# Kernel optimization log

Measured on AMD Instinct MI355X. Metric: run time of the kernel, lower is better.

The kernel has to match this reference:

```python
import jax, jax.numpy as jnp
import numpy as np

HIER_WEIGHT = 0.1

def setup_inputs() -> dict:
    key = jax.random.key(0)
    k1, k2, k3, k4, k5 = jax.random.split(key, 5)
    B, N, D = 128, 100000, 256
    E = N - 1
    return {
        "logits": jax.random.normal(k1, (B, N), dtype=jnp.float32),
        "labels": jax.random.randint(k2, (B,), 0, N, dtype=jnp.int64),
        "label_emb": jax.random.normal(k3, (N, D), dtype=jnp.float32),
        "parent_idx": jax.random.randint(k4, (E,), 0, N, dtype=jnp.int64),
        "child_idx": jax.random.randint(k5, (E,), 0, N, dtype=jnp.int64),
    }

def reference(logits, labels, label_emb, parent_idx, child_idx):
    # base loss: mean cross-entropy over the batch (loss_fn)
    logp = jax.nn.log_softmax(logits, axis=-1)                      # [B, N]
    ce = -jnp.take_along_axis(logp, labels[:, None], axis=-1)       # [B, 1]
    base_loss = jnp.mean(ce)
    # hierarchy penalty: sum over all (parent, child) edges of ||p - c||_2^2
    diff = label_emb[parent_idx] - label_emb[child_idx]             # [E, D]
    recursive_loss = jnp.sum(diff * diff)
    return base_loss + HIER_WEIGHT * recursive_loss
```

## Files before the change

kernel.cpp:

```cpp
#include <hip/hip_runtime.h>
#include <math.h>


#define TPB 256
#define WPB (TPB / 64)
#define EB  32
#define CE_SLICES 8

typedef float f32x4 __attribute__((ext_vector_type(4)));

__global__ __launch_bounds__(TPB, 4) void hier_work_kernel(
    const float* __restrict__ logits,
    const float* __restrict__ emb,
    const int* __restrict__ parent,
    const int* __restrict__ child,
    float* __restrict__ ws_edge,
    float* __restrict__ ws_ce,
    int N, int E, int n_edge_blocks)
{
    __shared__ float red[WPB];
    const int tid  = threadIdx.x;
    const int lane = tid & 63;
    const int wv   = tid >> 6;
    const float L2E = 1.4426950408889634f;

    if ((int)blockIdx.x < n_edge_blocks) {
        const int wave = blockIdx.x * WPB + wv;
        const int base = wave * EB;

        float acc = 0.0f;
        if (base < E) {
            const int n = min(EB, E - base);
            int idx = 0;
            if (lane < EB) {
                if (lane < n) idx = parent[base + lane];
            } else {
                const int j = lane - EB;
                if (j < n) idx = child[base + j];
            }
            const float4* __restrict__ emb4 = (const float4*)emb;

            #pragma unroll 4
            for (int j = 0; j < n; ++j) {
                const int p = __shfl(idx, j);
                const int c = __shfl(idx, j + EB);
                float4 a = emb4[(size_t)p * 64 + lane];
                float4 b = emb4[(size_t)c * 64 + lane];
                const float dx = a.x - b.x, dy = a.y - b.y;
                const float dz = a.z - b.z, dw = a.w - b.w;
                acc += dx * dx + dy * dy + dz * dz + dw * dw;
            }
        }

        #pragma unroll
        for (int off = 32; off; off >>= 1) acc += __shfl_xor(acc, off);
        if (lane == 0) red[wv] = acc;
        __syncthreads();
        if (tid == 0) {
            float t = 0.0f;
            #pragma unroll
            for (int k = 0; k < WPB; ++k) t += red[k];
            ws_edge[blockIdx.x] = t;
        }
    } else {
        const int cu    = (int)blockIdx.x - n_edge_blocks;
        const int row   = cu >> 3;
        const int slice = cu & (CE_SLICES - 1);
        const int n4    = N >> 2;
        const int per   = n4 / CE_SLICES;
        const f32x4* __restrict__ rp4 =
            (const f32x4*)(logits + (size_t)row * (size_t)N)
            + (size_t)slice * per;

        float s0 = 0.0f, s1 = 0.0f;
        int i = tid;
        for (; i + TPB < per; i += 2 * TPB) {
            f32x4 v0 = __builtin_nontemporal_load(&rp4[i]);
            f32x4 v1 = __builtin_nontemporal_load(&rp4[i + TPB]);
            s0 += exp2f(v0.x * L2E) + exp2f(v0.y * L2E)
                + exp2f(v0.z * L2E) + exp2f(v0.w * L2E);
            s1 += exp2f(v1.x * L2E) + exp2f(v1.y * L2E)
                + exp2f(v1.z * L2E) + exp2f(v1.w * L2E);
        }
        if (i < per) {
            f32x4 v = __builtin_nontemporal_load(&rp4[i]);
            s0 += exp2f(v.x * L2E) + exp2f(v.y * L2E)
                + exp2f(v.z * L2E) + exp2f(v.w * L2E);
        }
        if (slice == CE_SLICES - 1) {
            const int rem = N & 3;
            if (tid < rem) {
                const float* rp = logits + (size_t)row * (size_t)N;
                s0 += exp2f(rp[(size_t)(n4 << 2) + tid] * L2E);
            }
        }
        float s = s0 + s1;

        #pragma unroll
        for (int off = 32; off; off >>= 1) s += __shfl_xor(s, off);
        if (lane == 0) red[wv] = s;
        __syncthreads();
        if (tid == 0) {
            float t = 0.0f;
            #pragma unroll
            for (int k = 0; k < WPB; ++k) t += red[k];
            ws_ce[cu] = t;
        }
    }
}

__global__ __launch_bounds__(256) void finish_kernel(
    const float* __restrict__ logits, const int* __restrict__ labels,
    const float* __restrict__ ws_ce, const float* __restrict__ ws_edge,
    float* __restrict__ out, int B, int N, int n_edge_blocks)
{
    const int tid = threadIdx.x;
    float v = 0.0f;
    for (int r = tid; r < B; r += 256) {
        float s = 0.0f;
        #pragma unroll
        for (int k = 0; k < CE_SLICES; ++k) s += ws_ce[r * CE_SLICES + k];
        const int lab = labels[r];
        v += (logf(s) - logits[(size_t)r * (size_t)N + lab]) / (float)B;
    }
    float e = 0.0f;
    for (int i = tid; i < n_edge_blocks; i += 256) e += ws_edge[i];
    v += 0.1f * e;

    #pragma unroll
    for (int off = 32; off; off >>= 1) v += __shfl_xor(v, off);
    __shared__ float red[4];
    if ((tid & 63) == 0) red[tid >> 6] = v;
    __syncthreads();
    if (tid == 0) out[0] = red[0] + red[1] + red[2] + red[3];
}

extern "C" void kernel_launch(void* const* d_in, const int* in_sizes, int n_in,
                              void* d_out, int out_size, void* d_ws, size_t ws_size,
                              hipStream_t stream) {
    const float* logits = (const float*)d_in[0];
    const int*   labels = (const int*)d_in[1];
    const float* emb    = (const float*)d_in[2];
    const int*   parent = (const int*)d_in[3];
    const int*   child  = (const int*)d_in[4];
    float* out = (float*)d_out;

    const int B = in_sizes[1];
    const int N = in_sizes[0] / B;
    const int E = in_sizes[3];

    const int n_edge_waves  = (E + EB - 1) / EB;
    const int n_edge_blocks = (n_edge_waves + WPB - 1) / WPB;
    const int n_ce_blocks   = B * CE_SLICES;

    float* ws_edge = (float*)d_ws;
    float* ws_ce   = ws_edge + n_edge_blocks;

    hipLaunchKernelGGL(hier_work_kernel, dim3(n_edge_blocks + n_ce_blocks),
                       dim3(TPB), 0, stream,
                       logits, emb, parent, child, ws_edge, ws_ce,
                       N, E, n_edge_blocks);
    hipLaunchKernelGGL(finish_kernel, dim3(1), dim3(256), 0, stream,
                       logits, labels, ws_ce, ws_edge, out, B, N, n_edge_blocks);
}
```

Baseline: 44.33 us.

## Stage edge embedding gathers through LDS with double-buffered async loads

Full 32-edge waves now gather parent and child embedding rows through global_load_lds straight into a per-wave LDS ring buffer two deep. A vmcnt wait keeps two rows in flight while the previous pair is consumed. The goal is to overlap gather latency with compute without using vector registers for the loads. In exchange it adds 16 KB of LDS per block, which may limit occupancy, and a short two-deep pipeline may hide less latency than the old unrolled register loads. Partial waves keep the old path.

```diff
diff --git a/kernel.cpp b/kernel.cpp
--- a/kernel.cpp
+++ b/kernel.cpp
@@ -5,9 +5,17 @@
 #define TPB 256
 #define WPB (TPB / 64)
 #define EB  32
+#define DEPTH 2
 #define CE_SLICES 8
 
 typedef float f32x4 __attribute__((ext_vector_type(4)));
+
+#define GLOAD_LDS16(gsrc, ldst)                                              \
+    __builtin_amdgcn_global_load_lds(                                        \
+        (__attribute__((address_space(1))) void*)(size_t)(const void*)(gsrc),\
+        (__attribute__((address_space(3))) void*)(ldst), 16, 0, 0)
+
+#define VMCNT_WAIT(n) asm volatile("s_waitcnt vmcnt(" #n ")" ::: "memory")
 
 __global__ __launch_bounds__(TPB, 4) void hier_work_kernel(
     const float* __restrict__ logits,
@@ -18,6 +26,7 @@
     float* __restrict__ ws_ce,
     int N, int E, int n_edge_blocks)
 {
+    __shared__ __align__(16) float stage[WPB][DEPTH][2][256];
     __shared__ float red[WPB];
     const int tid  = threadIdx.x;
     const int lane = tid & 63;
@@ -38,17 +47,48 @@
                 const int j = lane - EB;
                 if (j < n) idx = child[base + j];
             }
-            const float4* __restrict__ emb4 = (const float4*)emb;
-
-            #pragma unroll 4
-            for (int j = 0; j < n; ++j) {
-                const int p = __shfl(idx, j);
-                const int c = __shfl(idx, j + EB);
-                float4 a = emb4[(size_t)p * 64 + lane];
-                float4 b = emb4[(size_t)c * 64 + lane];
-                const float dx = a.x - b.x, dy = a.y - b.y;
-                const float dz = a.z - b.z, dw = a.w - b.w;
-                acc += dx * dx + dy * dy + dz * dz + dw * dw;
+
+            if (n == EB) {
+#define ISSUE(jj) {                                                          \
+    const int p_ = __shfl(idx, (jj));                                        \
+    const int c_ = __shfl(idx, (jj) + EB);                                   \
+    GLOAD_LDS16(emb + ((size_t)p_ << 8) + (lane << 2),                       \
+                &stage[wv][(jj) & (DEPTH - 1)][0][0]);                       \
+    GLOAD_LDS16(emb + ((size_t)c_ << 8) + (lane << 2),                       \
+                &stage[wv][(jj) & (DEPTH - 1)][1][0]);                       \
+}
+#define CONSUME(jj) {                                                        \
+    const float4 a_ = *(const float4*)&stage[wv][(jj) & (DEPTH - 1)][0][lane << 2]; \
+    const float4 b_ = *(const float4*)&stage[wv][(jj) & (DEPTH - 1)][1][lane << 2]; \
+    const float dx_ = a_.x - b_.x, dy_ = a_.y - b_.y;                        \
+    const float dz_ = a_.z - b_.z, dw_ = a_.w - b_.w;                        \
+    acc += dx_ * dx_ + dy_ * dy_ + dz_ * dz_ + dw_ * dw_;                    \
+}
+                ISSUE(0)
+                ISSUE(1)
+                #pragma unroll
+                for (int j = 0; j < EB - 1; ++j) {
+                    VMCNT_WAIT(2);
+                    CONSUME(j);
+                    asm volatile("" ::: "memory");
+                    if (j + DEPTH < EB) ISSUE(j + DEPTH);
+                }
+                VMCNT_WAIT(0);
+                CONSUME(EB - 1);
+#undef ISSUE
+#undef CONSUME
+            } else {
+                const float4* __restrict__ emb4 = (const float4*)emb;
+                #pragma unroll 4
+                for (int j = 0; j < n; ++j) {
+                    const int p = __shfl(idx, j);
+                    const int c = __shfl(idx, j + EB);
+                    float4 a = emb4[(size_t)p * 64 + lane];
+                    float4 b = emb4[(size_t)c * 64 + lane];
+                    const float dx = a.x - b.x, dy = a.y - b.y;
+                    const float dz = a.z - b.z, dw = a.w - b.w;
+                    acc += dx * dx + dy * dy + dz * dz + dw * dw;
+                }
             }
         }
 
```

Result: slower. 47.02 us (+6.1%).
